# Kernel tuning notes

Hardware: AMD Instinct MI355X
Metric: run time of the kernel (lower is better)

Reference implementation:

```python
import jax, jax.numpy as jnp
import numpy as np

N = 50000        # total nodes (disjoint batch of graphs)
E = 800000       # total edges
F_IN = 8         # node feature dim
S = 6            # edge feature dim
H = 20           # ECC kernel-network hidden size (hidden_states)
N_OUT = 20       # ECC output channels (n_out=hidden_states)
G = 32           # GCN channels
D1 = 16          # first dense
N_GRAPHS = 512   # graphs in batch


def setup_inputs() -> dict:
    key = jax.random.key(0)
    ks = jax.random.split(key, 24)
    r = lambda k, sh, s: jax.random.normal(k, sh, dtype=jnp.float32) * s
    return {
        "x": r(ks[0], (N, F_IN), 1.0),
        "e": r(ks[1], (E, S), 1.0),
        "edge_index": jax.random.randint(ks[2], (2, E), 0, N, dtype=jnp.int32),
        "seg": jnp.sort(jax.random.randint(ks[3], (N,), 0, N_GRAPHS, dtype=jnp.int32)),
        # ECC kernel network: S -> H -> H -> F_IN*N_OUT
        "ecc_w1": r(ks[4], (S, H), 0.4), "ecc_b1": jnp.zeros((H,), jnp.float32),
        "ecc_w2": r(ks[5], (H, H), 0.2), "ecc_b2": jnp.zeros((H,), jnp.float32),
        "ecc_w3": r(ks[6], (H, F_IN * N_OUT), 0.2), "ecc_b3": jnp.zeros((F_IN * N_OUT,), jnp.float32),
        "ecc_root": r(ks[7], (F_IN, N_OUT), 0.3), "ecc_b": jnp.zeros((N_OUT,), jnp.float32),
        "gcn1_w": r(ks[8], (N_OUT, G), 0.2), "gcn1_b": jnp.zeros((G,), jnp.float32),
        "gcn2_w": r(ks[9], (G, G), 0.2), "gcn2_b": jnp.zeros((G,), jnp.float32),
        "d1_w": r(ks[10], (G, D1), 0.2), "d1_b": jnp.zeros((D1,), jnp.float32),
        "d2_w": r(ks[11], (D1, 1), 0.2), "d2_b": jnp.zeros((1,), jnp.float32),
    }


def reference(x, e, edge_index, seg,
              ecc_w1, ecc_b1, ecc_w2, ecc_b2, ecc_w3, ecc_b3, ecc_root, ecc_b,
              gcn1_w, gcn1_b, gcn2_w, gcn2_b, d1_w, d1_b, d2_w, d2_b):
    row, col = edge_index[0], edge_index[1]  # message col -> row

    # --- ECCConv: per-edge MLP produces an [F_IN, N_OUT] filter per edge ---
    h = jax.nn.relu(e @ ecc_w1 + ecc_b1)
    h = jax.nn.relu(h @ ecc_w2 + ecc_b2)
    w_edge = (h @ ecc_w3 + ecc_b3).reshape(E, F_IN, N_OUT)   # [E, F_in, F_out]
    msg = jnp.einsum('ef,efo->eo', x[col], w_edge)            # per-edge message
    agg = jax.ops.segment_sum(msg, row, num_segments=N)
    x1 = jax.nn.relu(agg + x @ ecc_root + ecc_b)              # root + bias + relu

    # --- GCN normalization from the edge list (A + I, symmetric norm) ---
    deg = jax.ops.segment_sum(jnp.ones((E,), x.dtype), row, num_segments=N) + 1.0
    dinv = jax.lax.rsqrt(deg)
    edge_norm = (dinv[row] * dinv[col])[:, None]
    self_norm = (dinv * dinv)[:, None]

    def gcn(hin, W, b):
        hw = hin @ W
        nmsg = jax.ops.segment_sum(edge_norm * hw[col], row, num_segments=N)
        return jax.nn.relu(nmsg + self_norm * hw + b)

    x2 = gcn(x1, gcn1_w, gcn1_b)
    x3 = gcn(x2, gcn2_w, gcn2_b)

    # --- GlobalSumPool over graph ids, then MLP head ---
    pooled = jax.ops.segment_sum(x3, seg, num_segments=N_GRAPHS)  # [n_graphs, G]
    out = (pooled @ d1_w + d1_b) @ d2_w + d2_b                    # [n_graphs, 1]
    return out
```

## Files before the change

kernel.cpp:

```cpp
#include <hip/hip_runtime.h>

#define S_DIM   6
#define H_DIM   20
#define F_INN   8
#define N_OUTC  20
#define G_DIM   32
#define D1_DIM  16
#define NGRAPH  512

typedef short short8 __attribute__((ext_vector_type(8)));
typedef float floatx4 __attribute__((ext_vector_type(4)));

__device__ __forceinline__ unsigned short f2bf(float f) {
    unsigned u = __float_as_uint(f);
    return (unsigned short)((u + 0x8000u) >> 16);
}
__device__ __forceinline__ float bf2f(unsigned short s) {
    return __uint_as_float(((unsigned)s) << 16);
}

__global__ __launch_bounds__(256) void loc_kernel(
    const int* __restrict__ ei, int E, int* __restrict__ cnt,
    int* __restrict__ loc)
{
    int i = blockIdx.x * 256 + threadIdx.x;
    if (i >= E) return;
    loc[i] = atomicAdd(&cnt[ei[i]], 1);
}

__global__ __launch_bounds__(256) void scanA_kernel(
    const int* __restrict__ deg, int N, int* __restrict__ bsum)
{
    int i = blockIdx.x * 256 + threadIdx.x;
    int v = (i < N) ? deg[i] : 0;
#pragma unroll
    for (int d = 1; d < 64; d <<= 1) v += __shfl_down(v, d, 64);
    __shared__ int ws[4];
    int wid = threadIdx.x >> 6;
    if ((threadIdx.x & 63) == 0) ws[wid] = v;
    __syncthreads();
    if (threadIdx.x == 0) bsum[blockIdx.x] = ws[0] + ws[1] + ws[2] + ws[3];
}

__global__ __launch_bounds__(256) void scanC_kernel(
    const int* __restrict__ deg, int N, const int* __restrict__ bsum, int nbl,
    int E, int* __restrict__ rowptr, float* __restrict__ dinv)
{
    __shared__ int ws[4];
    __shared__ int sboff;
    int t = threadIdx.x;
    {
        int v = (t < nbl && t < blockIdx.x) ? bsum[t] : 0;
#pragma unroll
        for (int d = 1; d < 64; d <<= 1) v += __shfl_down(v, d, 64);
        int wid = t >> 6;
        if ((t & 63) == 0) ws[wid] = v;
        __syncthreads();
        if (t == 0) sboff = ws[0] + ws[1] + ws[2] + ws[3];
        __syncthreads();
    }

    int i = blockIdx.x * 256 + t;
    int d0 = (i < N) ? deg[i] : 0;
    int v = d0;
#pragma unroll
    for (int d = 1; d < 64; d <<= 1) {
        int u = __shfl_up(v, d, 64);
        if ((t & 63) >= d) v += u;
    }
    __shared__ int ws2[4];
    int wid = t >> 6;
    if ((t & 63) == 63) ws2[wid] = v;
    __syncthreads();
    int woff = 0;
    for (int w = 0; w < wid; ++w) woff += ws2[w];
    if (i < N) {
        rowptr[i] = sboff + woff + v - d0;
        dinv[i] = rsqrtf((float)d0 + 1.0f);
    }
    if (blockIdx.x == 0 && t == 0) rowptr[N] = E;
}

__global__ __launch_bounds__(256) void build_kernel(
    const int* __restrict__ ei, int E, const float* __restrict__ e,
    const int* __restrict__ rowptr, const int* __restrict__ loc,
    float* __restrict__ e_sorted)
{
    int i = blockIdx.x * 256 + threadIdx.x;
    if (i >= E) return;
    int r = ei[i];
    int c = ei[E + i];
    int p = rowptr[r] + loc[i];

    const float2* ep = (const float2*)&e[(size_t)i * S_DIM];
    float2 e0 = ep[0], e1 = ep[1], e2 = ep[2];

    float4 r0, r1;
    r0.x = __int_as_float(c);
    r0.y = e0.x; r0.z = e0.y; r0.w = e1.x;
    r1.x = e1.y; r1.y = e2.x; r1.z = e2.y; r1.w = 0.0f;

    float4* dst = (float4*)&e_sorted[(size_t)p * 8];
    dst[0] = r0;
    dst[1] = r1;
}

__global__ __launch_bounds__(256) void ecc_mfma_kernel(
    const float* __restrict__ e_sorted, const float* __restrict__ x,
    const int* __restrict__ rowptr, int N, int E,
    const float* __restrict__ w1, const float* __restrict__ b1,
    const float* __restrict__ w2, const float* __restrict__ b2,
    const float* __restrict__ w3, const float* __restrict__ b3,
    float* __restrict__ agg, int* __restrict__ col_sorted)
{
    __shared__ char smem[26624];
    __shared__ int rbounds[2];
    unsigned short* Bl = (unsigned short*)smem;
    unsigned short (*h2b)[N_OUTC] = (unsigned short (*)[N_OUTC])(smem + 12288);
    unsigned short (*xb)[F_INN]   = (unsigned short (*)[F_INN])(smem + 22528);
    float* lmsg = (float*)smem;

    int t = threadIdx.x;
    int j0 = blockIdx.x * 256;
    int jend = min(j0 + 256, E);
    int j = j0 + t;

    if (t < 2) {
        int s = (t == 0) ? j0 : (jend - 1);
        int lo = 0, hi = N - 1;
        while (lo < hi) {
            int m = (lo + hi + 1) >> 1;
            if (rowptr[m] <= s) lo = m; else hi = m - 1;
        }
        rbounds[t] = lo;
    }

    for (int idx = t; idx < 6144; idx += 256) {
        int jj   = idx & 7;
        int n    = (idx >> 3) & 15;
        int quad = (idx >> 7) & 3;
        int nt   = (idx >> 9) & 1;
        int s    = idx >> 10;
        int K = 32 * s + quad * 8 + jj;
        int o = n + 16 * nt;
        float v = 0.0f;
        if (o < N_OUTC) {
            if (K < 160)      v = w3[(K >> 3) * 160 + (K & 7) * N_OUTC + o];
            else if (K < 168) v = b3[(K - 160) * N_OUTC + o];
        }
        Bl[idx] = f2bf(v);
    }

    if (j < E) {
        const float4* er = (const float4*)&e_sorted[(size_t)j * 8];
        float4 r0 = er[0], r1 = er[1];
        int c = __float_as_int(r0.x);
        col_sorted[j] = c;
        float ef[S_DIM] = {r0.y, r0.z, r0.w, r1.x, r1.y, r1.z};

        float h1[H_DIM];
#pragma unroll
        for (int jj = 0; jj < H_DIM; ++jj) {
            float a = b1[jj];
#pragma unroll
            for (int s = 0; s < S_DIM; ++s) a = fmaf(ef[s], w1[s * H_DIM + jj], a);
            h1[jj] = fmaxf(a, 0.0f);
        }

        float h2[H_DIM];
#pragma unroll
        for (int jj = 0; jj < H_DIM; ++jj) {
            float a = b2[jj];
#pragma unroll
            for (int k = 0; k < H_DIM; ++k) a = fmaf(h1[k], w2[k * H_DIM + jj], a);
            h2[jj] = fmaxf(a, 0.0f);
        }

        const float4* xp = (const float4*)&x[(size_t)c * F_INN];
        float4 xa = xp[0], xb4 = xp[1];
        float xf[F_INN] = {xa.x, xa.y, xa.z, xa.w, xb4.x, xb4.y, xb4.z, xb4.w};

#pragma unroll
        for (int o = 0; o < N_OUTC; ++o) h2b[t][o] = f2bf(h2[o]);
#pragma unroll
        for (int f = 0; f < F_INN; ++f) xb[t][f] = f2bf(xf[f]);
    } else {
#pragma unroll
        for (int o = 0; o < N_OUTC; ++o) h2b[t][o] = 0;
#pragma unroll
        for (int f = 0; f < F_INN; ++f) xb[t][f] = 0;
    }
    __syncthreads();

    int lane = t & 63;
    int quad = lane >> 4;
    int n = lane & 15;
    short8 Bf[12];
#pragma unroll
    for (int s = 0; s < 6; ++s)
#pragma unroll
        for (int nt = 0; nt < 2; ++nt)
            Bf[s * 2 + nt] = *(const short8*)&Bl[((((s * 2 + nt) * 4 + quad) * 16 + n) * 8)];

    int w = t >> 6;
    floatx4 acc0s[4], acc1s[4];
#pragma unroll
    for (int T = 0; T < 4; ++T) {
        int base = w * 64 + T * 16;
        int m = base + n;

        const short8 xv8 = *(const short8*)&xb[m][0];
        float xfl[F_INN];
#pragma unroll
        for (int jj = 0; jj < F_INN; ++jj) xfl[jj] = bf2f((unsigned short)xv8[jj]);

        floatx4 acc0 = {0.f, 0.f, 0.f, 0.f};
        floatx4 acc1 = {0.f, 0.f, 0.f, 0.f};
#pragma unroll
        for (int s = 0; s < 6; ++s) {
            short8 A = {0, 0, 0, 0, 0, 0, 0, 0};
            if (s < 5) {
                float h = bf2f(h2b[m][4 * s + quad]);
#pragma unroll
                for (int jj = 0; jj < F_INN; ++jj)
                    A[jj] = (short)f2bf(h * xfl[jj]);
            } else if (quad == 0) {
                A = xv8;
            }
            acc0 = __builtin_amdgcn_mfma_f32_16x16x32_bf16(A, Bf[s * 2 + 0], acc0, 0, 0, 0);
            acc1 = __builtin_amdgcn_mfma_f32_16x16x32_bf16(A, Bf[s * 2 + 1], acc1, 0, 0, 0);
        }
        acc0s[T] = acc0;
        acc1s[T] = acc1;
    }
    __syncthreads();

#pragma unroll
    for (int T = 0; T < 4; ++T) {
        int base = w * 64 + T * 16;
#pragma unroll
        for (int r = 0; r < 4; ++r) {
            int row = base + quad * 4 + r;
            lmsg[row * N_OUTC + n] = acc0s[T][r];
            if (n < 4) lmsg[row * N_OUTC + 16 + n] = acc1s[T][r];
        }
    }
    __syncthreads();

    int r0 = rbounds[0], r1 = rbounds[1];
    int work = (r1 - r0 + 1) * 5;
    for (int ww = t; ww < work; ww += 256) {
        int row = r0 + ww / 5;
        int q = ww - (ww / 5) * 5;
        int a0 = rowptr[row], a1 = rowptr[row + 1];
        int s0 = max(a0, j0), s1 = min(a1, jend);
        float4 acc = make_float4(0.f, 0.f, 0.f, 0.f);
        for (int s = s0; s < s1; ++s) {
            const float4 v = *(const float4*)&lmsg[(s - j0) * N_OUTC + q * 4];
            acc.x += v.x; acc.y += v.y; acc.z += v.z; acc.w += v.w;
        }
        float* dst = &agg[(size_t)row * N_OUTC + q * 4];
        if (a0 >= j0 && a1 <= jend) {
            *(float4*)dst = acc;
        } else {
            unsafeAtomicAdd(dst + 0, acc.x);
            unsafeAtomicAdd(dst + 1, acc.y);
            unsafeAtomicAdd(dst + 2, acc.z);
            unsafeAtomicAdd(dst + 3, acc.w);
        }
    }
}

__global__ __launch_bounds__(256) void node1_kernel(
    const float* __restrict__ agg, const float* __restrict__ x,
    const float* __restrict__ dinv, int N,
    const float* __restrict__ root, const float* __restrict__ eb,
    const float* __restrict__ g1w,
    unsigned short* __restrict__ hws1)
{
    int n = blockIdx.x * 256 + threadIdx.x;
    if (n >= N) return;

    const float4* xp = (const float4*)&x[(size_t)n * F_INN];
    float4 xa = xp[0], xb = xp[1];
    float xf[F_INN] = {xa.x, xa.y, xa.z, xa.w, xb.x, xb.y, xb.z, xb.w};

    float x1[N_OUTC];
#pragma unroll
    for (int o = 0; o < N_OUTC; ++o) {
        float a = agg[(size_t)n * N_OUTC + o] + eb[o];
#pragma unroll
        for (int f = 0; f < F_INN; ++f) a = fmaf(xf[f], root[f * N_OUTC + o], a);
        x1[o] = fmaxf(a, 0.0f);
    }

    float di = dinv[n];
#pragma unroll
    for (int q = 0; q < 4; ++q) {
        short8 o8;
#pragma unroll
        for (int u = 0; u < 8; ++u) {
            int g = q * 8 + u;
            float a = 0.0f;
#pragma unroll
            for (int o = 0; o < N_OUTC; ++o) a = fmaf(x1[o], g1w[o * G_DIM + g], a);
            o8[u] = (short)f2bf(a * di);
        }
        *(short8*)&hws1[(size_t)n * G_DIM + q * 8] = o8;
    }
}

template<bool DO_MATMUL>
__global__ __launch_bounds__(256) void gcn_gather_kernel(
    const unsigned short* __restrict__ hws, const int* __restrict__ rowptr,
    const int* __restrict__ col_sorted, const float* __restrict__ dinv, int N,
    const float* __restrict__ bias, const float* __restrict__ w2,
    unsigned short* __restrict__ outbuf)
{
    __shared__ float x2s[64][33];
    __shared__ float w2s[G_DIM * G_DIM];

    int t = threadIdx.x;
    int nl = t >> 2;
    int q = t & 3;
    int n = blockIdx.x * 64 + nl;

    if (DO_MATMUL) {
        ((float4*)w2s)[t] = ((const float4*)w2)[t];
    }

    float xo[8];
    float di = 0.0f;
    if (n < N) {
        di = dinv[n];
        int j0 = rowptr[n], j1 = rowptr[n + 1];
        short8 sv = *(const short8*)&hws[(size_t)n * G_DIM + q * 8];
        float s[8];
#pragma unroll
        for (int k = 0; k < 8; ++k) s[k] = bf2f((unsigned short)sv[k]);
        for (int j = j0; j < j1; ++j) {
            int c = col_sorted[j];
            short8 v = *(const short8*)&hws[(size_t)c * G_DIM + q * 8];
#pragma unroll
            for (int k = 0; k < 8; ++k) s[k] += bf2f((unsigned short)v[k]);
        }
#pragma unroll
        for (int k = 0; k < 8; ++k)
            xo[k] = fmaxf(fmaf(di, s[k], bias[q * 8 + k]), 0.0f);
    } else {
#pragma unroll
        for (int k = 0; k < 8; ++k) xo[k] = 0.0f;
    }

    if (DO_MATMUL) {
#pragma unroll
        for (int k = 0; k < 8; ++k) x2s[nl][q * 8 + k] = xo[k];
        __syncthreads();
        if (n < N) {
            float a[8];
#pragma unroll
            for (int k = 0; k < 8; ++k) a[k] = 0.0f;
#pragma unroll
            for (int g = 0; g < G_DIM; ++g) {
                float xv = x2s[nl][g];
#pragma unroll
                for (int k = 0; k < 8; ++k)
                    a[k] = fmaf(xv, w2s[g * G_DIM + q * 8 + k], a[k]);
            }
            short8 o8;
#pragma unroll
            for (int k = 0; k < 8; ++k) o8[k] = (short)f2bf(a[k] * di);
            *(short8*)&outbuf[(size_t)n * G_DIM + q * 8] = o8;
        }
    } else {
        if (n < N) {
            short8 o8;
#pragma unroll
            for (int k = 0; k < 8; ++k) o8[k] = (short)f2bf(xo[k]);
            *(short8*)&outbuf[(size_t)n * G_DIM + q * 8] = o8;
        }
    }
}

__global__ __launch_bounds__(256) void pool_head_kernel(
    const unsigned short* __restrict__ x3, const int* __restrict__ seg, int N,
    const float* __restrict__ d1w, const float* __restrict__ d1b,
    const float* __restrict__ d2w, const float* __restrict__ d2b,
    float* __restrict__ out)
{
    __shared__ float red[8][G_DIM];
    __shared__ float pvec[G_DIM];
    __shared__ int bounds[2];
    int g = blockIdx.x;
    int t = threadIdx.x;
    if (t < 2) {
        int target = g + t;
        int lo = 0, hi = N;
        while (lo < hi) {
            int m = (lo + hi) >> 1;
            if (seg[m] < target) lo = m + 1; else hi = m;
        }
        bounds[t] = lo;
    }
    __syncthreads();
    int n0 = bounds[0], n1 = bounds[1];
    int ch = t & (G_DIM - 1);
    int slice = t >> 5;
    float a = 0.0f;
    for (int n = n0 + slice; n < n1; n += 8)
        a += bf2f(x3[(size_t)n * G_DIM + ch]);
    red[slice][ch] = a;
    __syncthreads();
    if (slice == 0) {
        float s = red[0][ch];
#pragma unroll
        for (int k = 1; k < 8; ++k) s += red[k][ch];
        pvec[ch] = s;
    }
    __syncthreads();
    if (t < 64) {
        float acc = 0.0f;
        if (t < D1_DIM) {
            float tj = d1b[t];
#pragma unroll
            for (int gg = 0; gg < G_DIM; ++gg)
                tj = fmaf(pvec[gg], d1w[gg * D1_DIM + t], tj);
            acc = tj * d2w[t];
        }
#pragma unroll
        for (int d = 1; d < D1_DIM; d <<= 1) acc += __shfl_down(acc, d, 64);
        if (t == 0) out[g] = acc + d2b[0];
    }
}

extern "C" void kernel_launch(void* const* d_in, const int* in_sizes, int n_in,
                              void* d_out, int out_size, void* d_ws, size_t ws_size,
                              hipStream_t stream)
{
    const float* x    = (const float*)d_in[0];
    const float* e    = (const float*)d_in[1];
    const int*   ei   = (const int*)d_in[2];
    const int*   seg  = (const int*)d_in[3];
    const float* w1   = (const float*)d_in[4];
    const float* b1   = (const float*)d_in[5];
    const float* w2   = (const float*)d_in[6];
    const float* b2   = (const float*)d_in[7];
    const float* w3   = (const float*)d_in[8];
    const float* b3   = (const float*)d_in[9];
    const float* root = (const float*)d_in[10];
    const float* eb   = (const float*)d_in[11];
    const float* g1w  = (const float*)d_in[12];
    const float* g1b  = (const float*)d_in[13];
    const float* g2w  = (const float*)d_in[14];
    const float* g2b  = (const float*)d_in[15];
    const float* d1w  = (const float*)d_in[16];
    const float* d1b  = (const float*)d_in[17];
    const float* d2w  = (const float*)d_in[18];
    const float* d2b  = (const float*)d_in[19];

    const int N = in_sizes[3];
    const int E = in_sizes[1] / S_DIM;
    float* out = (float*)d_out;

    const int nbl = (N + 255) / 256;
    const int ebl = (E + 255) / 256;

    char* ws = (char*)d_ws;
    size_t off = 0;
    auto alloc = [&](size_t elems) -> char* {
        char* p = ws + off;
        off += ((elems * 4 + 15) & ~(size_t)15);
        return p;
    };
    int*   cnt        = (int*)  alloc(N);
    float* agg        = (float*)alloc((size_t)N * N_OUTC);
    size_t zero_bytes = off;
    int*   rowptr     = (int*)  alloc(N + 1);
    int*   bsum       = (int*)  alloc(nbl);
    float* dinv       = (float*)alloc(N);
    int*   loc        = (int*)  alloc(E);
    int*   col_sorted = (int*)  alloc(E);
    float* e_sorted   = (float*)alloc((size_t)E * 8);
    unsigned short* hws1 = (unsigned short*)alloc((size_t)N * G_DIM / 2);
    unsigned short* hws2 = (unsigned short*)alloc((size_t)N * G_DIM / 2);
    unsigned short* x3   = (unsigned short*)alloc((size_t)N * G_DIM / 2);
    (void)ws_size;

    hipMemsetAsync(d_ws, 0, zero_bytes, stream);

    loc_kernel<<<ebl, 256, 0, stream>>>(ei, E, cnt, loc);
    scanA_kernel<<<nbl, 256, 0, stream>>>(cnt, N, bsum);
    scanC_kernel<<<nbl, 256, 0, stream>>>(cnt, N, bsum, nbl, E, rowptr, dinv);
    build_kernel<<<ebl, 256, 0, stream>>>(ei, E, e, rowptr, loc, e_sorted);
    ecc_mfma_kernel<<<ebl, 256, 0, stream>>>(e_sorted, x, rowptr, N, E,
                                             w1, b1, w2, b2, w3, b3,
                                             agg, col_sorted);
    node1_kernel<<<nbl, 256, 0, stream>>>(agg, x, dinv, N, root, eb, g1w, hws1);
    gcn_gather_kernel<true><<<(N + 63) / 64, 256, 0, stream>>>(
        hws1, rowptr, col_sorted, dinv, N, g1b, g2w, hws2);
    gcn_gather_kernel<false><<<(N + 63) / 64, 256, 0, stream>>>(
        hws2, rowptr, col_sorted, dinv, N, g2b, nullptr, x3);
    pool_head_kernel<<<NGRAPH, 256, 0, stream>>>(x3, seg, N, d1w, d1b, d2w, d2b, out);
}
```

Measured before the change: 277.1 us.

## Precompute bf16 filter weights once and pack sorted edge records as bf16

The bf16 MFMA B-operand layout of w3/b3 is now built once by a small prep kernel and read straight from global memory. Previously each ECC block rebuilt it in shared memory. Sorted edge records shrink from 32 to 16 bytes by storing the six edge features as packed bf16 next to the column index. This cuts per-block setup work, shared memory use and edge-record traffic, at the cost of rounding the edge features to bf16 before the first MLP layer.

```diff
diff --git a/kernel.cpp b/kernel.cpp
--- a/kernel.cpp
+++ b/kernel.cpp
@@ -19,6 +19,27 @@
     return __uint_as_float(((unsigned)s) << 16);
 }
 
+__global__ __launch_bounds__(256) void prep_kernel(
+    const float* __restrict__ w3, const float* __restrict__ b3,
+    unsigned short* __restrict__ B3f)
+{
+    int idx = blockIdx.x * 256 + threadIdx.x;
+    if (idx >= 6144) return;
+    int jj   = idx & 7;
+    int n    = (idx >> 3) & 15;
+    int quad = (idx >> 7) & 3;
+    int nt   = (idx >> 9) & 1;
+    int s    = idx >> 10;
+    int K = 32 * s + quad * 8 + jj;
+    int o = n + 16 * nt;
+    float v = 0.0f;
+    if (o < N_OUTC) {
+        if (K < 160)      v = w3[(K >> 3) * 160 + (K & 7) * N_OUTC + o];
+        else if (K < 168) v = b3[(K - 160) * N_OUTC + o];
+    }
+    B3f[idx] = f2bf(v);
+}
+
 __global__ __launch_bounds__(256) void loc_kernel(
     const int* __restrict__ ei, int E, int* __restrict__ cnt,
     int* __restrict__ loc)
@@ -84,7 +105,7 @@
 __global__ __launch_bounds__(256) void build_kernel(
     const int* __restrict__ ei, int E, const float* __restrict__ e,
     const int* __restrict__ rowptr, const int* __restrict__ loc,
-    float* __restrict__ e_sorted)
+    int4* __restrict__ e_sorted)
 {
     int i = blockIdx.x * 256 + threadIdx.x;
     if (i >= E) return;
@@ -95,29 +116,26 @@
     const float2* ep = (const float2*)&e[(size_t)i * S_DIM];
     float2 e0 = ep[0], e1 = ep[1], e2 = ep[2];
 
-    float4 r0, r1;
-    r0.x = __int_as_float(c);
-    r0.y = e0.x; r0.z = e0.y; r0.w = e1.x;
-    r1.x = e1.y; r1.y = e2.x; r1.z = e2.y; r1.w = 0.0f;
-
-    float4* dst = (float4*)&e_sorted[(size_t)p * 8];
-    dst[0] = r0;
-    dst[1] = r1;
+    int4 rec;
+    rec.x = c;
+    rec.y = (int)f2bf(e0.x) | ((int)f2bf(e0.y) << 16);
+    rec.z = (int)f2bf(e1.x) | ((int)f2bf(e1.y) << 16);
+    rec.w = (int)f2bf(e2.x) | ((int)f2bf(e2.y) << 16);
+    e_sorted[p] = rec;
 }
 
 __global__ __launch_bounds__(256) void ecc_mfma_kernel(
-    const float* __restrict__ e_sorted, const float* __restrict__ x,
+    const int4* __restrict__ e_sorted, const float* __restrict__ x,
     const int* __restrict__ rowptr, int N, int E,
+    const unsigned short* __restrict__ B3f,
     const float* __restrict__ w1, const float* __restrict__ b1,
     const float* __restrict__ w2, const float* __restrict__ b2,
-    const float* __restrict__ w3, const float* __restrict__ b3,
     float* __restrict__ agg, int* __restrict__ col_sorted)
 {
-    __shared__ char smem[26624];
+    __shared__ char smem[20480];
     __shared__ int rbounds[2];
-    unsigned short* Bl = (unsigned short*)smem;
-    unsigned short (*h2b)[N_OUTC] = (unsigned short (*)[N_OUTC])(smem + 12288);
-    unsigned short (*xb)[F_INN]   = (unsigned short (*)[F_INN])(smem + 22528);
+    unsigned short (*h2b)[N_OUTC] = (unsigned short (*)[N_OUTC])smem;
+    unsigned short (*xb)[F_INN]   = (unsigned short (*)[F_INN])(smem + 10240);
     float* lmsg = (float*)smem;
 
     int t = threadIdx.x;
@@ -135,28 +153,18 @@
         rbounds[t] = lo;
     }
 
-    for (int idx = t; idx < 6144; idx += 256) {
-        int jj   = idx & 7;
-        int n    = (idx >> 3) & 15;
-        int quad = (idx >> 7) & 3;
-        int nt   = (idx >> 9) & 1;
-        int s    = idx >> 10;
-        int K = 32 * s + quad * 8 + jj;
-        int o = n + 16 * nt;
-        float v = 0.0f;
-        if (o < N_OUTC) {
-            if (K < 160)      v = w3[(K >> 3) * 160 + (K & 7) * N_OUTC + o];
-            else if (K < 168) v = b3[(K - 160) * N_OUTC + o];
-        }
-        Bl[idx] = f2bf(v);
-    }
-
     if (j < E) {
-        const float4* er = (const float4*)&e_sorted[(size_t)j * 8];
-        float4 r0 = er[0], r1 = er[1];
-        int c = __float_as_int(r0.x);
+        int4 rec = e_sorted[j];
+        int c = rec.x;
         col_sorted[j] = c;
-        float ef[S_DIM] = {r0.y, r0.z, r0.w, r1.x, r1.y, r1.z};
+        float ef[S_DIM] = {
+            bf2f((unsigned short)(rec.y & 0xffff)),
+            bf2f((unsigned short)((unsigned)rec.y >> 16)),
+            bf2f((unsigned short)(rec.z & 0xffff)),
+            bf2f((unsigned short)((unsigned)rec.z >> 16)),
+            bf2f((unsigned short)(rec.w & 0xffff)),
+            bf2f((unsigned short)((unsigned)rec.w >> 16))
+        };
 
         float h1[H_DIM];
 #pragma unroll
@@ -195,12 +203,13 @@
     int lane = t & 63;
     int quad = lane >> 4;
     int n = lane & 15;
+    const short8* Bg = (const short8*)B3f;
     short8 Bf[12];
 #pragma unroll
     for (int s = 0; s < 6; ++s)
 #pragma unroll
         for (int nt = 0; nt < 2; ++nt)
-            Bf[s * 2 + nt] = *(const short8*)&Bl[((((s * 2 + nt) * 4 + quad) * 16 + n) * 8)];
+            Bf[s * 2 + nt] = Bg[((s * 2 + nt) * 4 + quad) * 16 + n];
 
     int w = t >> 6;
     floatx4 acc0s[4], acc1s[4];
@@ -480,7 +489,8 @@
     float* dinv       = (float*)alloc(N);
     int*   loc        = (int*)  alloc(E);
     int*   col_sorted = (int*)  alloc(E);
-    float* e_sorted   = (float*)alloc((size_t)E * 8);
+    unsigned short* B3f = (unsigned short*)alloc(6144 / 2);
+    int4*  e_sorted   = (int4*) alloc((size_t)E * 4);
     unsigned short* hws1 = (unsigned short*)alloc((size_t)N * G_DIM / 2);
     unsigned short* hws2 = (unsigned short*)alloc((size_t)N * G_DIM / 2);
     unsigned short* x3   = (unsigned short*)alloc((size_t)N * G_DIM / 2);
@@ -488,13 +498,13 @@
 
     hipMemsetAsync(d_ws, 0, zero_bytes, stream);
 
+    prep_kernel<<<24, 256, 0, stream>>>(w3, b3, B3f);
     loc_kernel<<<ebl, 256, 0, stream>>>(ei, E, cnt, loc);
     scanA_kernel<<<nbl, 256, 0, stream>>>(cnt, N, bsum);
     scanC_kernel<<<nbl, 256, 0, stream>>>(cnt, N, bsum, nbl, E, rowptr, dinv);
     build_kernel<<<ebl, 256, 0, stream>>>(ei, E, e, rowptr, loc, e_sorted);
-    ecc_mfma_kernel<<<ebl, 256, 0, stream>>>(e_sorted, x, rowptr, N, E,
-                                             w1, b1, w2, b2, w3, b3,
-                                             agg, col_sorted);
+    ecc_mfma_kernel<<<ebl, 256, 0, stream>>>(e_sorted, x, rowptr, N, E, B3f,
+                                             w1, b1, w2, b2, agg, col_sorted);
     node1_kernel<<<nbl, 256, 0, stream>>>(agg, x, dinv, N, root, eb, g1w, hws1);
     gcn_gather_kernel<true><<<(N + 63) / 64, 256, 0, stream>>>(
         hws1, rowptr, col_sorted, dinv, N, g1b, g2w, hws2);
```

After: 269.7 us. 2.7% less time.
